# Kernel tuning notes

Hardware: AMD Instinct MI355X
Metric: run time of the kernel (lower is better)

## Reference

```python
import jax, jax.numpy as jnp
import numpy as np

NBITS = 4
OUT_F = 2048
IN_F = 2048


def _bit_ste(w, nbits):
    # clamp to [-1,1], quantize magnitude to nbits levels, keep sign
    step = float(2 ** nbits - 1)
    w = jnp.clip(w, -1.0, 1.0)
    return jnp.round(jnp.abs(w) * step) / step * jnp.sign(w)


def setup_inputs() -> dict:
    key = jax.random.key(0)
    ks = jax.random.split(key, 6)
    ex = np.arange(NBITS - 1, -1, -1)
    exps = jnp.asarray(2.0 ** ex / (2.0 ** NBITS - 1), dtype=jnp.float32)
    inp = {
        "input": jax.random.normal(ks[0], (8, 2048, IN_F), dtype=jnp.float32),
        # bit-plane weights: sigmoid of these gives soft bits in (0,1)
        "pweight": jax.random.normal(ks[1], (OUT_F, IN_F, NBITS), dtype=jnp.float32),
        "nweight": jax.random.normal(ks[2], (OUT_F, IN_F, NBITS), dtype=jnp.float32),
        "exps": exps,
        "bexps": exps,
        "mask_weight": jnp.ones((NBITS,), dtype=jnp.float32),  # init.constant_(1)
        "scale": jnp.array([0.05], dtype=jnp.float32),
        "pbias": jax.random.uniform(ks[3], (OUT_F, NBITS), dtype=jnp.float32, minval=0.0, maxval=float(2 ** NBITS - 1)) // 1.0 % 2.0,
        "nbias": jax.random.uniform(ks[4], (OUT_F, NBITS), dtype=jnp.float32, minval=0.0, maxval=float(2 ** NBITS - 1)) // 1.0 % 2.0,
        "biasscale": jnp.array([0.05], dtype=jnp.float32),
    }
    return inp


def reference(input, pweight, nweight, exps, bexps, mask_weight, scale, pbias, nbias, biasscale):
    temp = 1.0
    # temp_s and mask_discrete are all-ones buffers -> identity factors
    mask = jax.nn.sigmoid(mask_weight)                      # [N]
    soft = jax.nn.sigmoid(temp * pweight) - jax.nn.sigmoid(temp * nweight)  # [O,I,N]
    weight = jnp.einsum('oin,n->oi', soft, exps * mask) * scale[0]          # [O,I]
    bias_raw = jnp.einsum('on,n->o', pbias - nbias, bexps)  # [O]
    bias = _bit_ste(bias_raw, NBITS) * biasscale[0]
    # F.linear: y = x @ W^T + b
    return jnp.einsum('bsi,oi->bso', input, weight) + bias
```

## Files before the change

### kernel.cpp

```cpp
#include <hip/hip_runtime.h>
#include <hip/hip_bf16.h>
#include <stdint.h>

#define M_DIM 16384
#define N_DIM 2048
#define K_DIM 2048

typedef __attribute__((ext_vector_type(8))) __bf16 bf16x8;
typedef __attribute__((ext_vector_type(4))) float f32x4;

__device__ __forceinline__ unsigned short f2bf(float f) {
  unsigned int u = __builtin_bit_cast(unsigned int, f);
  u += 0x7FFFu + ((u >> 16) & 1u);
  return (unsigned short)(u >> 16);
}

__device__ __forceinline__ float sigmoidf_(float x) {
  return 1.0f / (1.0f + __expf(-x));
}

__global__ __launch_bounds__(256) void convert_x(const float4* __restrict__ x,
                                                 uint4* __restrict__ xb) {
  int idx = blockIdx.x * 256 + threadIdx.x;
  float4 a = x[idx * 2];
  float4 b = x[idx * 2 + 1];
  uint4 r;
  r.x = (unsigned)f2bf(a.x) | ((unsigned)f2bf(a.y) << 16);
  r.y = (unsigned)f2bf(a.z) | ((unsigned)f2bf(a.w) << 16);
  r.z = (unsigned)f2bf(b.x) | ((unsigned)f2bf(b.y) << 16);
  r.w = (unsigned)f2bf(b.z) | ((unsigned)f2bf(b.w) << 16);
  xb[idx] = r;
}

__global__ __launch_bounds__(256) void make_w(const float4* __restrict__ pw,
                                              const float4* __restrict__ nw,
                                              const float* __restrict__ exps,
                                              const float* __restrict__ maskw,
                                              const float* __restrict__ scale,
                                              unsigned short* __restrict__ wout) {
  int idx = blockIdx.x * 256 + threadIdx.x;
  float4 p = pw[idx];
  float4 n = nw[idx];
  float s = scale[0];
  float c0 = sigmoidf_(maskw[0]) * exps[0] * s;
  float c1 = sigmoidf_(maskw[1]) * exps[1] * s;
  float c2 = sigmoidf_(maskw[2]) * exps[2] * s;
  float c3 = sigmoidf_(maskw[3]) * exps[3] * s;
  float w = (sigmoidf_(p.x) - sigmoidf_(n.x)) * c0
          + (sigmoidf_(p.y) - sigmoidf_(n.y)) * c1
          + (sigmoidf_(p.z) - sigmoidf_(n.z)) * c2
          + (sigmoidf_(p.w) - sigmoidf_(n.w)) * c3;
  wout[idx] = f2bf(w);
}

__global__ __launch_bounds__(256) void make_bias(const float* __restrict__ pb,
                                                 const float* __restrict__ nb,
                                                 const float* __restrict__ bexps,
                                                 const float* __restrict__ bscale,
                                                 float* __restrict__ bias) {
  int o = blockIdx.x * 256 + threadIdx.x;
  if (o < N_DIM) {
    float x = 0.f;
#pragma unroll
    for (int n = 0; n < 4; ++n) x += (pb[o * 4 + n] - nb[o * 4 + n]) * bexps[n];
    float xc = fminf(fmaxf(x, -1.f), 1.f);
    float mag = rintf(fabsf(xc) * 15.f) * (1.f / 15.f);
    float sgn = (xc > 0.f) ? 1.f : ((xc < 0.f) ? -1.f : 0.f);
    bias[o] = mag * sgn * bscale[0];
  }
}

#define TM 128
#define TN 128
#define BK 32

__device__ __forceinline__ void gload16(const void* g, void* l) {
  __builtin_amdgcn_global_load_lds(
      (const __attribute__((address_space(1))) unsigned int*)g,
      (__attribute__((address_space(3))) unsigned int*)l, 16, 0, 0);
}

__global__ __launch_bounds__(256) void gemm_bias(const unsigned short* __restrict__ X,
                                                 const unsigned short* __restrict__ W,
                                                 const float* __restrict__ bias,
                                                 float* __restrict__ out) {
  __shared__ unsigned short As[TM * BK];
  __shared__ unsigned short Bs[TN * BK];
  const int tid = threadIdx.x;
  const int bm = blockIdx.y, bn = blockIdx.x;
  const int row0 = bm * TM, col0 = bn * TN;
  const int w = tid >> 6, l = tid & 63;
  const int wr = (w >> 1) * 64;
  const int wc = (w & 1) * 64;
  const int lr = l & 15;
  const int lk = (l >> 4) * 8;

  const int srow = tid >> 2;
  const int scol = (tid & 3) * 8;
  const unsigned short* gA0 = X + (size_t)(row0 + srow) * K_DIM + scol;
  const unsigned short* gA1 = X + (size_t)(row0 + 64 + srow) * K_DIM + scol;
  const unsigned short* gB0 = W + (size_t)(col0 + srow) * K_DIM + scol;
  const unsigned short* gB1 = W + (size_t)(col0 + 64 + srow) * K_DIM + scol;

  f32x4 acc[4][4] = {};

  for (int k0 = 0; k0 < K_DIM; k0 += BK) {
    gload16(gA0 + k0, &As[tid * 8]);
    gload16(gA1 + k0, &As[64 * BK + tid * 8]);
    gload16(gB0 + k0, &Bs[tid * 8]);
    gload16(gB1 + k0, &Bs[64 * BK + tid * 8]);
    __syncthreads();

    bf16x8 a[4], b[4];
#pragma unroll
    for (int m = 0; m < 4; ++m)
      a[m] = *(const bf16x8*)&As[(wr + m * 16 + lr) * BK + lk];
#pragma unroll
    for (int n = 0; n < 4; ++n)
      b[n] = *(const bf16x8*)&Bs[(wc + n * 16 + lr) * BK + lk];
#pragma unroll
    for (int m = 0; m < 4; ++m)
#pragma unroll
      for (int n = 0; n < 4; ++n)
        acc[m][n] = __builtin_amdgcn_mfma_f32_16x16x32_bf16(a[m], b[n], acc[m][n], 0, 0, 0);
    __syncthreads();
  }

  float bv[4];
#pragma unroll
  for (int n = 0; n < 4; ++n) bv[n] = bias[col0 + wc + n * 16 + lr];
  const int orow = (l >> 4) * 4;
#pragma unroll
  for (int m = 0; m < 4; ++m) {
#pragma unroll
    for (int n = 0; n < 4; ++n) {
      const int colg = col0 + wc + n * 16 + lr;
#pragma unroll
      for (int r = 0; r < 4; ++r) {
        int rowg = row0 + wr + m * 16 + orow + r;
        out[(size_t)rowg * N_DIM + colg] = acc[m][n][r] + bv[n];
      }
    }
  }
}

extern "C" void kernel_launch(void* const* d_in, const int* in_sizes, int n_in,
                              void* d_out, int out_size, void* d_ws, size_t ws_size,
                              hipStream_t stream) {
  const float* input  = (const float*)d_in[0];
  const float* pweight = (const float*)d_in[1];
  const float* nweight = (const float*)d_in[2];
  const float* exps   = (const float*)d_in[3];
  const float* bexps  = (const float*)d_in[4];
  const float* maskw  = (const float*)d_in[5];
  const float* scale  = (const float*)d_in[6];
  const float* pbias  = (const float*)d_in[7];
  const float* nbias  = (const float*)d_in[8];
  const float* bscale = (const float*)d_in[9];
  float* out = (float*)d_out;

  unsigned short* Xb = (unsigned short*)d_ws;
  unsigned short* Wb = (unsigned short*)((char*)d_ws + (size_t)M_DIM * K_DIM * 2);
  float* bias = (float*)((char*)d_ws + (size_t)M_DIM * K_DIM * 2 + (size_t)N_DIM * K_DIM * 2);

  convert_x<<<(M_DIM * (size_t)K_DIM) / 8 / 256, 256, 0, stream>>>((const float4*)input, (uint4*)Xb);
  make_w<<<((size_t)N_DIM * K_DIM) / 256, 256, 0, stream>>>(
      (const float4*)pweight, (const float4*)nweight, exps, maskw, scale, Wb);
  make_bias<<<(N_DIM + 255) / 256, 256, 0, stream>>>(pbias, nbias, bexps, bscale, bias);

  dim3 grid(N_DIM / TN, M_DIM / TM);
  gemm_bias<<<grid, 256, 0, stream>>>(Xb, Wb, bias, out);
}
```

Before: 238.2 us.

## Rewrite GEMM with 256x256 tiles, double-buffered swizzled LDS and phased MFMA pipeline

Replaces the 128x128 single-buffered GEMM with a 256x256 tile, BK=64, 512-thread kernel. Global-to-LDS loads for the next k-tile are double-buffered and interleaved with four MFMA phases using explicit vmcnt waits and barriers. LDS uses an XOR swizzle to avoid bank conflicts, and block indices are remapped for L2 locality. The aim is to hide memory latency and raise arithmetic intensity. In exchange it needs much more LDS and many more registers per thread, and the hand-tuned waitcnt sequencing is fragile.

After: 205.3 us. -13.8%, faster.

```diff
diff --git a/kernel.cpp b/kernel.cpp
--- a/kernel.cpp
+++ b/kernel.cpp
@@ -70,9 +70,11 @@
   }
 }
 
-#define TM 128
-#define TN 128
-#define BK 32
+
+#define BM 256
+#define BN 256
+#define BK 64
+#define NT (K_DIM / BK)
 
 __device__ __forceinline__ void gload16(const void* g, void* l) {
   __builtin_amdgcn_global_load_lds(
@@ -80,68 +82,148 @@
       (__attribute__((address_space(3))) unsigned int*)l, 16, 0, 0);
 }
 
-__global__ __launch_bounds__(256) void gemm_bias(const unsigned short* __restrict__ X,
-                                                 const unsigned short* __restrict__ W,
-                                                 const float* __restrict__ bias,
-                                                 float* __restrict__ out) {
-  __shared__ unsigned short As[TM * BK];
-  __shared__ unsigned short Bs[TN * BK];
+#define VMCNT(n) asm volatile("s_waitcnt vmcnt(" #n ")" ::: "memory")
+#define BAR() __builtin_amdgcn_s_barrier()
+
+__global__ __launch_bounds__(512, 2) void gemm_bias(const unsigned short* __restrict__ X,
+                                                    const unsigned short* __restrict__ W,
+                                                    const float* __restrict__ bias,
+                                                    float* __restrict__ out) {
+  __shared__ unsigned short sA[2][BM * BK];
+  __shared__ unsigned short sB[2][BN * BK];
+
   const int tid = threadIdx.x;
-  const int bm = blockIdx.y, bn = blockIdx.x;
-  const int row0 = bm * TM, col0 = bn * TN;
+  const int swz = ((int)blockIdx.x & 7) * 64 + ((int)blockIdx.x >> 3);
+  const int bm = swz >> 3;
+  const int bn = swz & 7;
+  const int row0 = bm * BM, col0 = bn * BN;
+
   const int w = tid >> 6, l = tid & 63;
-  const int wr = (w >> 1) * 64;
-  const int wc = (w & 1) * 64;
+  const int wr = w >> 2;
+  const int wc = w & 3;
   const int lr = l & 15;
-  const int lk = (l >> 4) * 8;
-
-  const int srow = tid >> 2;
-  const int scol = (tid & 3) * 8;
-  const unsigned short* gA0 = X + (size_t)(row0 + srow) * K_DIM + scol;
-  const unsigned short* gA1 = X + (size_t)(row0 + 64 + srow) * K_DIM + scol;
-  const unsigned short* gB0 = W + (size_t)(col0 + srow) * K_DIM + scol;
-  const unsigned short* gB1 = W + (size_t)(col0 + 64 + srow) * K_DIM + scol;
-
-  f32x4 acc[4][4] = {};
-
-  for (int k0 = 0; k0 < K_DIM; k0 += BK) {
-    gload16(gA0 + k0, &As[tid * 8]);
-    gload16(gA1 + k0, &As[64 * BK + tid * 8]);
-    gload16(gB0 + k0, &Bs[tid * 8]);
-    gload16(gB1 + k0, &Bs[64 * BK + tid * 8]);
-    __syncthreads();
-
-    bf16x8 a[4], b[4];
-#pragma unroll
-    for (int m = 0; m < 4; ++m)
-      a[m] = *(const bf16x8*)&As[(wr + m * 16 + lr) * BK + lk];
-#pragma unroll
-    for (int n = 0; n < 4; ++n)
-      b[n] = *(const bf16x8*)&Bs[(wc + n * 16 + lr) * BK + lk];
-#pragma unroll
-    for (int m = 0; m < 4; ++m)
-#pragma unroll
-      for (int n = 0; n < 4; ++n)
-        acc[m][n] = __builtin_amdgcn_mfma_f32_16x16x32_bf16(a[m], b[n], acc[m][n], 0, 0, 0);
-    __syncthreads();
+  const int lk4 = l >> 4;
+  const int l7 = l & 7;
+
+  const unsigned short* Ag = X + (size_t)row0 * K_DIM;
+  const unsigned short* Bg = W + (size_t)col0 * K_DIM;
+
+  const int srl = (tid >> 3) & 31;
+  const int sc16 = (tid & 7) ^ ((tid >> 3) & 7);
+  const int shi = tid >> 8;
+  const int slin = ((tid >> 3) & 24) * 64 + (tid & 63) * 8;
+
+  auto stage = [&](unsigned short* lbase, const unsigned short* gbase,
+                   int rb0, int rb1, int tk) {
+    int rb = shi ? rb1 : rb0;
+    int trow = rb + srl;
+    gload16(gbase + (size_t)trow * K_DIM + tk * BK + sc16 * 8,
+            lbase + rb * 64 + slin);
+  };
+
+  auto rdA = [&](const unsigned short* base, int mf, int ks) -> bf16x8 {
+    int trow = wr * 128 + mf * 16 + lr;
+    int c16l = (ks * 4 + lk4) ^ l7;
+    return *(const bf16x8*)&base[trow * 64 + c16l * 8];
+  };
+  auto rdB = [&](const unsigned short* base, int nf, int ks) -> bf16x8 {
+    int trow = wc * 64 + nf * 16 + lr;
+    int c16l = (ks * 4 + lk4) ^ l7;
+    return *(const bf16x8*)&base[trow * 64 + c16l * 8];
+  };
+
+  f32x4 acc[8][4] = {};
+  bf16x8 a[4][2], b[4][2];
+
+#define PHASE_MFMA(mh, nh)                                                    \
+  __builtin_amdgcn_s_setprio(1);                                              \
+  _Pragma("unroll") for (int i = 0; i < 4; ++i)                               \
+  _Pragma("unroll") for (int j = 0; j < 2; ++j)                               \
+  _Pragma("unroll") for (int ks = 0; ks < 2; ++ks)                            \
+      acc[(mh) * 4 + i][(nh) * 2 + j] = __builtin_amdgcn_mfma_f32_16x16x32_bf16( \
+          a[i][ks], b[(nh) * 2 + j][ks], acc[(mh) * 4 + i][(nh) * 2 + j], 0, 0, 0); \
+  __builtin_amdgcn_s_setprio(0);
+
+  {
+    unsigned short* qa = sA[0];
+    unsigned short* qb = sB[0];
+    stage(qa, Ag, 0, 32, 0);
+    stage(qa, Ag, 128, 160, 0);
+    stage(qb, Bg, 0, 64, 0);
+    stage(qb, Bg, 128, 192, 0);
+    stage(qb, Bg, 32, 96, 0);
+    stage(qb, Bg, 160, 224, 0);
+    stage(qa, Ag, 64, 96, 0);
+    stage(qa, Ag, 192, 224, 0);
+  }
+  VMCNT(4);
+  BAR();
+
+  for (int t = 0; t < NT; ++t) {
+    const int p = t & 1, q = p ^ 1;
+    const bool last = (t == NT - 1);
+    const unsigned short* pa = sA[p];
+    const unsigned short* pb = sB[p];
+    unsigned short* qa = sA[q];
+    unsigned short* qb = sB[q];
+
+#pragma unroll
+    for (int i = 0; i < 4; ++i)
+#pragma unroll
+      for (int ks = 0; ks < 2; ++ks) a[i][ks] = rdA(pa, i, ks);
+#pragma unroll
+    for (int j = 0; j < 2; ++j)
+#pragma unroll
+      for (int ks = 0; ks < 2; ++ks) b[j][ks] = rdB(pb, j, ks);
+    if (!last) { stage(qa, Ag, 0, 32, t + 1); stage(qa, Ag, 128, 160, t + 1); }
+    BAR();
+    PHASE_MFMA(0, 0);
+    if (!last) { VMCNT(4); } else { VMCNT(2); }
+    BAR();
+
+#pragma unroll
+    for (int j = 2; j < 4; ++j)
+#pragma unroll
+      for (int ks = 0; ks < 2; ++ks) b[j][ks] = rdB(pb, j, ks);
+    if (!last) { stage(qb, Bg, 0, 64, t + 1); stage(qb, Bg, 128, 192, t + 1); }
+    BAR();
+    PHASE_MFMA(0, 1);
+    if (!last) { VMCNT(4); } else { VMCNT(0); }
+    BAR();
+
+#pragma unroll
+    for (int i = 0; i < 4; ++i)
+#pragma unroll
+      for (int ks = 0; ks < 2; ++ks) a[i][ks] = rdA(pa, 4 + i, ks);
+    if (!last) { stage(qb, Bg, 32, 96, t + 1); stage(qb, Bg, 160, 224, t + 1); }
+    BAR();
+    PHASE_MFMA(1, 0);
+    BAR();
+
+    if (!last) { stage(qa, Ag, 64, 96, t + 1); stage(qa, Ag, 192, 224, t + 1); }
+    BAR();
+    PHASE_MFMA(1, 1);
+    if (!last) { VMCNT(4); }
+    BAR();
   }
 
   float bv[4];
 #pragma unroll
-  for (int n = 0; n < 4; ++n) bv[n] = bias[col0 + wc + n * 16 + lr];
-  const int orow = (l >> 4) * 4;
-#pragma unroll
-  for (int m = 0; m < 4; ++m) {
-#pragma unroll
-    for (int n = 0; n < 4; ++n) {
-      const int colg = col0 + wc + n * 16 + lr;
+  for (int nf = 0; nf < 4; ++nf) bv[nf] = bias[col0 + wc * 64 + nf * 16 + lr];
+  const int orow = lk4 * 4;
+#pragma unroll
+  for (int mf = 0; mf < 8; ++mf) {
+#pragma unroll
+    for (int nf = 0; nf < 4; ++nf) {
+      const int colg = col0 + wc * 64 + nf * 16 + lr;
 #pragma unroll
       for (int r = 0; r < 4; ++r) {
-        int rowg = row0 + wr + m * 16 + orow + r;
-        out[(size_t)rowg * N_DIM + colg] = acc[m][n][r] + bv[n];
+        int rowg = row0 + wr * 128 + mf * 16 + orow + r;
+        out[(size_t)rowg * N_DIM + colg] = acc[mf][nf][r] + bv[nf];
       }
     }
   }
+#undef PHASE_MFMA
 }
 
 extern "C" void kernel_launch(void* const* d_in, const int* in_sizes, int n_in,
@@ -168,6 +250,6 @@
       (const float4*)pweight, (const float4*)nweight, exps, maskw, scale, Wb);
   make_bias<<<(N_DIM + 255) / 256, 256, 0, stream>>>(pbias, nbias, bexps, bscale, bias);
 
-  dim3 grid(N_DIM / TN, M_DIM / TM);
-  gemm_bias<<<grid, 256, 0, stream>>>(Xb, Wb, bias, out);
-}
+  dim3 grid((M_DIM / BM) * (N_DIM / BN));
+  gemm_bias<<<grid, 512, 0, stream>>>(Xb, Wb, bias, out);
+}
```
